# Kernel optimization log

Hardware: AMD Instinct MI355X
Metric: run time of the kernel (lower is better)

## Reference

```python
import jax, jax.numpy as jnp
import numpy as np

VOCAB = 100000
EMB = 128
WINDOW = 200
N_T = 64
B = 128
N_W = 128
ALPHA = 0.5
PAD = VOCAB - 1


def setup_inputs() -> dict:
    key = jax.random.key(0)
    ks = jax.random.split(key, 8)
    s = 0.5 / EMB
    tvecs = jax.random.uniform(ks[0], (VOCAB, EMB), minval=-s, maxval=s).at[PAD].set(0.0)
    cvecs = jax.random.uniform(ks[1], (VOCAB, EMB), minval=-s, maxval=s).at[PAD].set(0.0)
    W_w = jax.random.normal(ks[2], (N_W, 2 * EMB)) * 0.02
    W_b = jnp.zeros((N_W,))
    h_w = jax.random.normal(ks[3], (1, N_W)) * 0.02
    h_b = jnp.zeros((1,))
    batch_titems = jax.random.randint(ks[4], (B, N_T), 0, VOCAB)
    batch_citems = jax.random.randint(ks[5], (B, WINDOW), 0, VOCAB)
    mask_pad_ids = jax.random.randint(ks[6], (B, WINDOW), 0, 2).astype(bool)
    return {
        "tvecs": tvecs, "cvecs": cvecs,
        "W_w": W_w, "W_b": W_b, "h_w": h_w, "h_b": h_b,
        "batch_titems": batch_titems, "batch_citems": batch_citems,
        "mask_pad_ids": mask_pad_ids,
    }


def reference(tvecs, cvecs, W_w, W_b, h_w, h_b, batch_titems, batch_citems, mask_pad_ids):
    q = tvecs[batch_titems]   # (B, N_T, E)  target-item (query) embeddings
    k = cvecs[batch_citems]   # (B, W, E)    context-item (key/value) embeddings
    # W(concat(p, q)) == p @ Wp.T + q @ Wq.T + b  -- split weight, avoid the
    # materialized (B, N_T, W, 2E) repeat+cat tensor of the torch code.
    Wp, Wq = W_w[:, :EMB], W_w[:, EMB:]
    hp = jnp.einsum('bte,ne->btn', q, Wp)   # (B, N_T, N_W)
    hq = jnp.einsum('bwe,ne->bwn', k, Wq)   # (B, W,  N_W)
    hidden = jax.nn.relu(hp[:, :, None, :] + hq[:, None, :, :] + W_b)  # (B,N_T,W,N_W)
    att = jnp.einsum('btwn,n->btw', hidden, h_w[0]) + h_b[0]            # (B,N_T,W)
    att = jnp.where(mask_pad_ids[:, None, :], -jnp.inf, att)
    att = jax.nn.softmax(att, axis=-1)
    out = jnp.einsum('btw,bwe->bte', att, k)                            # (B,N_T,E)
    norm = (1000.0 - mask_pad_ids.sum(axis=1).astype(out.dtype)) ** ALPHA  # (B,)
    return out / norm[:, None, None]
```

## Files before the change

kernel.cpp:

```cpp
#include <hip/hip_runtime.h>
#include <math.h>

#define EMB 128
#define WIN 200
#define NT 64
#define BB 128
#define WPAD 208

typedef short bf16x8 __attribute__((ext_vector_type(8)));
typedef float f32x4  __attribute__((ext_vector_type(4)));

__device__ __forceinline__ unsigned pk2bf16(float a, float b) {
    unsigned ua = __float_as_uint(a), ub = __float_as_uint(b);
    ua = (ua + 0x7FFFu + ((ua >> 16) & 1u)) >> 16;
    ub = (ub + 0x7FFFu + ((ub >> 16) & 1u)) >> 16;
    return ua | (ub << 16);
}
__device__ __forceinline__ float rdlane(float v, int l) {
    return __uint_as_float(__builtin_amdgcn_readlane(__float_as_uint(v), l));
}

__global__ __launch_bounds__(256, 4) void proj_kernel(
    const float* __restrict__ tvecs, const float* __restrict__ cvecs,
    const int* __restrict__ titems, const int* __restrict__ citems,
    const float* __restrict__ Ww, const float* __restrict__ Wbias,
    const int* __restrict__ mi, int* __restrict__ flag,
    float* __restrict__ hp_out, float* __restrict__ hqT_out)
{
    __shared__ __align__(16) ushort s_A[64 * 128];
    __shared__ __align__(16) ushort s_B[128 * 128];
    __shared__ float s_bias[128];
    __shared__ int   sdet;

    const int tid = threadIdx.x;

    if (blockIdx.x == 528) {
        if (tid == 0) sdet = 0;
        __syncthreads();
        int bad = 0;
        for (int i = tid; i < 6400; i += 256)
            if ((unsigned)mi[i] > 1u) bad = 1;
        if (bad) sdet = 1;
        __syncthreads();
        if (tid == 0) flag[0] = sdet;
        return;
    }

    const bool is_hp = blockIdx.x < 128;
    const float* table = is_hp ? tvecs : cvecs;
    const int*   idx   = is_hp ? titems : citems;
    const int  rbase = (is_hp ? blockIdx.x : (blockIdx.x - 128)) * 64;
    const int  eoff  = is_hp ? 0 : EMB;

    if (tid < 128) s_bias[tid] = Wbias[tid];

    for (int i = tid; i < 2048; i += 256) {
        int row = i >> 5, j = i & 31;
        float4 v = *(const float4*)&table[(size_t)idx[rbase + row] * 128 + 4 * j];
        uint2 p; p.x = pk2bf16(v.x, v.y); p.y = pk2bf16(v.z, v.w);
        *(uint2*)((char*)s_A + row * 256 + (((j >> 1) ^ (row & 7)) << 4) + (j & 1) * 8) = p;
    }
    for (int i = tid; i < 4096; i += 256) {
        int n = i >> 5, j = i & 31;
        float4 v = *(const float4*)&Ww[n * 256 + eoff + 4 * j];
        uint2 p; p.x = pk2bf16(v.x, v.y); p.y = pk2bf16(v.z, v.w);
        *(uint2*)((char*)s_B + n * 256 + (((j >> 1) ^ (n & 7)) << 4) + (j & 1) * 8) = p;
    }
    __syncthreads();

    const int wid = tid >> 6, l = tid & 63;
    const int rl = l & 15, kg = l >> 4;
    const int r0 = wid * 16;

    f32x4 acc[8];
#pragma unroll
    for (int i = 0; i < 8; ++i) acc[i] = (f32x4){0.f, 0.f, 0.f, 0.f};

    const int arow = r0 + rl;
#pragma unroll
    for (int s = 0; s < 4; ++s) {
        bf16x8 af = *(const bf16x8*)((const char*)s_A
                        + arow * 256 + ((((s << 2) + kg) ^ (arow & 7)) << 4));
#pragma unroll
        for (int nt = 0; nt < 8; ++nt) {
            int bn = nt * 16 + rl;
            bf16x8 bfr = *(const bf16x8*)((const char*)s_B
                            + bn * 256 + ((((s << 2) + kg) ^ (bn & 7)) << 4));
            acc[nt] = __builtin_amdgcn_mfma_f32_16x16x32_bf16(af, bfr, acc[nt], 0, 0, 0);
        }
    }

#pragma unroll
    for (int i = 0; i < 4; ++i) {
        int ri = rbase + r0 + kg * 4 + i;
        if (is_hp) {
            size_t base = (size_t)ri * 128;
#pragma unroll
            for (int nt = 0; nt < 8; ++nt)
                hp_out[base + nt * 16 + rl] = acc[nt][i];
        } else {
            int b2 = ri / 200;
            int wl = ri - b2 * 200;
#pragma unroll
            for (int nt = 0; nt < 8; ++nt) {
                int col = nt * 16 + rl;
                hqT_out[(((size_t)b2 * 32 + (col >> 2)) * WPAD + wl) * 4 + (col & 3)]
                    = acc[nt][i] + s_bias[col];
            }
        }
    }
}

__global__ __launch_bounds__(512, 2) void attn_kernel(
    const float* __restrict__ cvecs, const int* __restrict__ citems,
    const void* __restrict__ mask_raw, const int* __restrict__ flagp,
    const float* __restrict__ hwg, const float* __restrict__ hp,
    const float* __restrict__ hqT, float* __restrict__ outp)
{
    __shared__ __align__(16) float4 s_hq4[32 * 128];
    __shared__ __align__(16) float4 s_k4[128 * 32];
    __shared__ __align__(16) float  s_hp[32 * 128];
    __shared__ __align__(16) float  s_hw[128];
    __shared__ int s_ci[WIN];
    __shared__ int s_widx[WIN];
    __shared__ int s_m;

    const int tid  = threadIdx.x;
    const int b    = blockIdx.x >> 1;
    const int tb   = (blockIdx.x & 1) * 32;
    const int lane = tid & 63;
    const int wid  = tid >> 6;
    const int t0   = wid * 4;

    for (int i = tid; i < 1024; i += 512) {
        int t = i >> 5, e4 = i & 31;
        *(float4*)&s_hp[t * 128 + e4 * 4] =
            *(const float4*)&hp[((size_t)(b * 64 + tb + t)) * 128 + e4 * 4];
    }
    if (tid < 128) s_hw[tid] = hwg[tid];
    if (tid < WIN) s_ci[tid] = citems[b * WIN + tid];
    if (wid == 0) {
        const int boolmode = flagp[0];
        const unsigned char* mb = (const unsigned char*)mask_raw;
        const int*           mi = (const int*)mask_raw;
        int base = 0;
#pragma unroll
        for (int r = 0; r < 4; ++r) {
            int w  = r * 64 + lane;
            int mv = 1;
            if (w < WIN) mv = boolmode ? (int)mb[b * WIN + w] : mi[b * WIN + w];
            unsigned long long act = __ballot(mv == 0);
            if (mv == 0)
                s_widx[base + __popcll(act & ((1ull << lane) - 1ull))] = w;
            base += __popcll(act);
        }
        if (lane == 0) s_m = base;
    }
    __syncthreads();

    const int m = s_m;
    const float invn = 1.f / sqrtf(800.f + (float)m);
    size_t orow = ((size_t)(b * 64 + tb + t0)) * 128;

    if (m == 0) {
#pragma unroll
        for (int j = 0; j < 4; ++j)
            *(float2*)&outp[orow + (size_t)j * 128 + lane * 2] = make_float2(0.f, 0.f);
        return;
    }

    const float4* hq4  = (const float4*)hqT + (size_t)b * 32 * WPAD;
    const float4* hp4a = (const float4*)&s_hp[t0 * 128];
    const float4* hw4p = (const float4*)s_hw;
    const float4* cv4  = (const float4*)cvecs;

#define SC(J, K, HV, P)                                                        \
    va[J][K] += hwv.x * fmaxf(HV.x + P.x, 0.f) + hwv.y * fmaxf(HV.y + P.y, 0.f)\
              + hwv.z * fmaxf(HV.z + P.z, 0.f) + hwv.w * fmaxf(HV.w + P.w, 0.f);

    if (m <= 128) {
        {
            const int w2 = tid & 127, nc0 = tid >> 7;
            if (w2 < m) {
                const int wi = s_widx[w2];
#pragma unroll
                for (int nc = nc0; nc < 32; nc += 4)
                    s_hq4[nc * 128 + w2] = hq4[(size_t)nc * WPAD + wi];
            }
            const int e4 = tid & 31, w0 = tid >> 5;
            for (int w2k = w0; w2k < m; w2k += 16) {
                int ci = s_ci[s_widx[w2k]];
                s_k4[w2k * 32 + e4] = cv4[(size_t)ci * 32 + e4];
            }
        }
        __syncthreads();

        float va[4][2];
#pragma unroll
        for (int j = 0; j < 4; ++j) { va[j][0] = 0.f; va[j][1] = 0.f; }

#pragma unroll 2
        for (int nc = 0; nc < 32; ++nc) {
            float4 hv0 = s_hq4[nc * 128 + lane];
            float4 hv1 = s_hq4[nc * 128 + 64 + lane];
            float4 hwv = hw4p[nc];
            float4 p0  = hp4a[0 * 32 + nc];
            float4 p1  = hp4a[1 * 32 + nc];
            float4 p2  = hp4a[2 * 32 + nc];
            float4 p3  = hp4a[3 * 32 + nc];
            SC(0, 0, hv0, p0) SC(0, 1, hv1, p0)
            SC(1, 0, hv0, p1) SC(1, 1, hv1, p1)
            SC(2, 0, hv0, p2) SC(2, 1, hv1, p2)
            SC(3, 0, hv0, p3) SC(3, 1, hv1, p3)
        }

#pragma unroll
        for (int j = 0; j < 4; ++j) {
            float mx = -1e30f;
#pragma unroll
            for (int kt = 0; kt < 2; ++kt) {
                float v = (kt * 64 + lane < m) ? va[j][kt] : -1e30f;
                va[j][kt] = v;
                mx = fmaxf(mx, v);
            }
#pragma unroll
            for (int off = 32; off; off >>= 1) mx = fmaxf(mx, __shfl_xor(mx, off));
            float sum = 0.f;
#pragma unroll
            for (int kt = 0; kt < 2; ++kt) {
                float e = (va[j][kt] <= -1e29f) ? 0.f : __expf(va[j][kt] - mx);
                va[j][kt] = e;
                sum += e;
            }
#pragma unroll
            for (int off = 32; off; off >>= 1) sum += __shfl_xor(sum, off);
            float is = 1.f / sum;
            va[j][0] *= is; va[j][1] *= is;
        }

        float2 po[4];
#pragma unroll
        for (int j = 0; j < 4; ++j) po[j] = make_float2(0.f, 0.f);
        const float2* s_k2 = (const float2*)s_k4;
#pragma unroll
        for (int kt = 0; kt < 2; ++kt) {
            if (kt * 64 < m) {
                const int wn = min(64, m - kt * 64);
                for (int w = 0; w < wn; ++w) {
                    float2 kv = s_k2[(kt * 64 + w) * 64 + lane];
                    float a0 = rdlane(va[0][kt], w);
                    float a1 = rdlane(va[1][kt], w);
                    float a2 = rdlane(va[2][kt], w);
                    float a3 = rdlane(va[3][kt], w);
                    po[0].x += a0 * kv.x; po[0].y += a0 * kv.y;
                    po[1].x += a1 * kv.x; po[1].y += a1 * kv.y;
                    po[2].x += a2 * kv.x; po[2].y += a2 * kv.y;
                    po[3].x += a3 * kv.x; po[3].y += a3 * kv.y;
                }
            }
        }
#pragma unroll
        for (int j = 0; j < 4; ++j)
            *(float2*)&outp[orow + (size_t)j * 128 + lane * 2] =
                make_float2(po[j].x * invn, po[j].y * invn);
    } else {
        int wreg[4];
        const int mc = m - 1;
#pragma unroll
        for (int kt = 0; kt < 4; ++kt)
            wreg[kt] = s_widx[min(kt * 64 + lane, mc)];

        float va[4][4];
#pragma unroll
        for (int j = 0; j < 4; ++j)
#pragma unroll
            for (int k = 0; k < 4; ++k) va[j][k] = 0.f;

#pragma unroll 2
        for (int nc = 0; nc < 32; ++nc) {
            const float4* base = hq4 + (size_t)nc * WPAD;
            float4 hv0 = base[wreg[0]];
            float4 hv1 = base[wreg[1]];
            float4 hv2 = base[wreg[2]];
            float4 hv3 = base[wreg[3]];
            float4 hwv = hw4p[nc];
            float4 p0  = hp4a[0 * 32 + nc];
            float4 p1  = hp4a[1 * 32 + nc];
            float4 p2  = hp4a[2 * 32 + nc];
            float4 p3  = hp4a[3 * 32 + nc];
            SC(0, 0, hv0, p0) SC(0, 1, hv1, p0) SC(0, 2, hv2, p0) SC(0, 3, hv3, p0)
            SC(1, 0, hv0, p1) SC(1, 1, hv1, p1) SC(1, 2, hv2, p1) SC(1, 3, hv3, p1)
            SC(2, 0, hv0, p2) SC(2, 1, hv1, p2) SC(2, 2, hv2, p2) SC(2, 3, hv3, p2)
            SC(3, 0, hv0, p3) SC(3, 1, hv1, p3) SC(3, 2, hv2, p3) SC(3, 3, hv3, p3)
        }

#pragma unroll
        for (int j = 0; j < 4; ++j) {
            float mx = -1e30f;
#pragma unroll
            for (int kt = 0; kt < 4; ++kt) {
                float v = (kt * 64 + lane < m) ? va[j][kt] : -1e30f;
                va[j][kt] = v;
                mx = fmaxf(mx, v);
            }
#pragma unroll
            for (int off = 32; off; off >>= 1) mx = fmaxf(mx, __shfl_xor(mx, off));
            float sum = 0.f;
#pragma unroll
            for (int kt = 0; kt < 4; ++kt) {
                float e = (va[j][kt] <= -1e29f) ? 0.f : __expf(va[j][kt] - mx);
                va[j][kt] = e;
                sum += e;
            }
#pragma unroll
            for (int off = 32; off; off >>= 1) sum += __shfl_xor(sum, off);
            float is = 1.f / sum;
#pragma unroll
            for (int kt = 0; kt < 4; ++kt) va[j][kt] *= is;
        }

        float2 po[4];
#pragma unroll
        for (int j = 0; j < 4; ++j) po[j] = make_float2(0.f, 0.f);
        const char* cvb = (const char*)cvecs;
#pragma unroll
        for (int kt = 0; kt < 4; ++kt) {
            if (kt * 64 < m) {
                const int wn = min(64, m - kt * 64);
                for (int w = 0; w < wn; ++w) {
                    unsigned off = (unsigned)s_ci[s_widx[kt * 64 + w]] * 512u;
                    float2 kv = *(const float2*)(cvb + off + lane * 8);
                    float a0 = rdlane(va[0][kt], w);
                    float a1 = rdlane(va[1][kt], w);
                    float a2 = rdlane(va[2][kt], w);
                    float a3 = rdlane(va[3][kt], w);
                    po[0].x += a0 * kv.x; po[0].y += a0 * kv.y;
                    po[1].x += a1 * kv.x; po[1].y += a1 * kv.y;
                    po[2].x += a2 * kv.x; po[2].y += a2 * kv.y;
                    po[3].x += a3 * kv.x; po[3].y += a3 * kv.y;
                }
            }
        }
#pragma unroll
        for (int j = 0; j < 4; ++j)
            *(float2*)&outp[orow + (size_t)j * 128 + lane * 2] =
                make_float2(po[j].x * invn, po[j].y * invn);
    }
#undef SC
}

extern "C" void kernel_launch(void* const* d_in, const int* in_sizes, int n_in,
                              void* d_out, int out_size, void* d_ws, size_t ws_size,
                              hipStream_t stream) {
    const float* tvecs = (const float*)d_in[0];
    const float* cvecs = (const float*)d_in[1];
    const float* Ww    = (const float*)d_in[2];
    const float* Wb    = (const float*)d_in[3];
    const float* hw    = (const float*)d_in[4];
    const int* titems  = (const int*)d_in[6];
    const int* citems  = (const int*)d_in[7];
    const void* mask   = d_in[8];
    float* out         = (float*)d_out;

    const size_t needed = (size_t)(64 + (size_t)BB * NT * 128
                                   + (size_t)BB * 32 * WPAD * 4) * 4;
    if (ws_size < needed) return;

    int*   flag   = (int*)d_ws;
    float* hp_ws  = (float*)d_ws + 64;
    float* hqT_ws = hp_ws + (size_t)BB * NT * 128;

    proj_kernel<<<529, 256, 0, stream>>>(tvecs, cvecs, titems, citems,
                                         Ww, Wb, (const int*)mask, flag,
                                         hp_ws, hqT_ws);
    attn_kernel<<<BB * 2, 512, 0, stream>>>(cvecs, citems, mask, flag,
                                            hw, hp_ws, hqT_ws, out);
}
```

Baseline: 51.99 us.

## Store projection intermediates and staged keys as bf16, enlarge proj blocks

The projection outputs hp and hqT are now written to workspace as bf16 instead of fp32. The attention kernel reads them as bf16, stages context key vectors in shared memory as bf16, and unpacks everything to fp32 for the math. The projection kernel moves to 512-thread blocks that each handle 128 rows, and the attention kernel's launch bounds are raised to 4 blocks. This halves intermediate memory traffic and LDS use to allow more occupancy, but adds rounding error in the scores and the output.

```diff
diff --git a/kernel.cpp b/kernel.cpp
--- a/kernel.cpp
+++ b/kernel.cpp
@@ -10,35 +10,41 @@
 typedef short bf16x8 __attribute__((ext_vector_type(8)));
 typedef float f32x4  __attribute__((ext_vector_type(4)));
 
+__device__ __forceinline__ ushort bf16r(float x) {
+    unsigned u = __float_as_uint(x);
+    return (ushort)((u + 0x7FFFu + ((u >> 16) & 1u)) >> 16);
+}
 __device__ __forceinline__ unsigned pk2bf16(float a, float b) {
     unsigned ua = __float_as_uint(a), ub = __float_as_uint(b);
     ua = (ua + 0x7FFFu + ((ua >> 16) & 1u)) >> 16;
     ub = (ub + 0x7FFFu + ((ub >> 16) & 1u)) >> 16;
     return ua | (ub << 16);
 }
+__device__ __forceinline__ float bf_lo(unsigned u) { return __uint_as_float(u << 16); }
+__device__ __forceinline__ float bf_hi(unsigned u) { return __uint_as_float(u & 0xFFFF0000u); }
 __device__ __forceinline__ float rdlane(float v, int l) {
     return __uint_as_float(__builtin_amdgcn_readlane(__float_as_uint(v), l));
 }
 
-__global__ __launch_bounds__(256, 4) void proj_kernel(
+__global__ __launch_bounds__(512, 4) void proj_kernel(
     const float* __restrict__ tvecs, const float* __restrict__ cvecs,
     const int* __restrict__ titems, const int* __restrict__ citems,
     const float* __restrict__ Ww, const float* __restrict__ Wbias,
     const int* __restrict__ mi, int* __restrict__ flag,
-    float* __restrict__ hp_out, float* __restrict__ hqT_out)
+    ushort* __restrict__ hp_out, ushort* __restrict__ hqT_out)
 {
-    __shared__ __align__(16) ushort s_A[64 * 128];
+    __shared__ __align__(16) ushort s_A[128 * 128];
     __shared__ __align__(16) ushort s_B[128 * 128];
     __shared__ float s_bias[128];
     __shared__ int   sdet;
 
     const int tid = threadIdx.x;
 
-    if (blockIdx.x == 528) {
+    if (blockIdx.x == 264) {
         if (tid == 0) sdet = 0;
         __syncthreads();
         int bad = 0;
-        for (int i = tid; i < 6400; i += 256)
+        for (int i = tid; i < 6400; i += 512)
             if ((unsigned)mi[i] > 1u) bad = 1;
         if (bad) sdet = 1;
         __syncthreads();
@@ -46,21 +52,21 @@
         return;
     }
 
-    const bool is_hp = blockIdx.x < 128;
+    const bool is_hp = blockIdx.x < 64;
     const float* table = is_hp ? tvecs : cvecs;
     const int*   idx   = is_hp ? titems : citems;
-    const int  rbase = (is_hp ? blockIdx.x : (blockIdx.x - 128)) * 64;
+    const int  rbase = (is_hp ? blockIdx.x : (blockIdx.x - 64)) * 128;
     const int  eoff  = is_hp ? 0 : EMB;
 
     if (tid < 128) s_bias[tid] = Wbias[tid];
 
-    for (int i = tid; i < 2048; i += 256) {
+    for (int i = tid; i < 4096; i += 512) {
         int row = i >> 5, j = i & 31;
         float4 v = *(const float4*)&table[(size_t)idx[rbase + row] * 128 + 4 * j];
         uint2 p; p.x = pk2bf16(v.x, v.y); p.y = pk2bf16(v.z, v.w);
         *(uint2*)((char*)s_A + row * 256 + (((j >> 1) ^ (row & 7)) << 4) + (j & 1) * 8) = p;
     }
-    for (int i = tid; i < 4096; i += 256) {
+    for (int i = tid; i < 4096; i += 512) {
         int n = i >> 5, j = i & 31;
         float4 v = *(const float4*)&Ww[n * 256 + eoff + 4 * j];
         uint2 p; p.x = pk2bf16(v.x, v.y); p.y = pk2bf16(v.z, v.w);
@@ -97,7 +103,7 @@
             size_t base = (size_t)ri * 128;
 #pragma unroll
             for (int nt = 0; nt < 8; ++nt)
-                hp_out[base + nt * 16 + rl] = acc[nt][i];
+                hp_out[base + nt * 16 + rl] = bf16r(acc[nt][i]);
         } else {
             int b2 = ri / 200;
             int wl = ri - b2 * 200;
@@ -105,22 +111,22 @@
             for (int nt = 0; nt < 8; ++nt) {
                 int col = nt * 16 + rl;
                 hqT_out[(((size_t)b2 * 32 + (col >> 2)) * WPAD + wl) * 4 + (col & 3)]
-                    = acc[nt][i] + s_bias[col];
-            }
-        }
-    }
-}
-
-__global__ __launch_bounds__(512, 2) void attn_kernel(
+                    = bf16r(acc[nt][i] + s_bias[col]);
+            }
+        }
+    }
+}
+
+__global__ __launch_bounds__(512, 4) void attn_kernel(
     const float* __restrict__ cvecs, const int* __restrict__ citems,
     const void* __restrict__ mask_raw, const int* __restrict__ flagp,
-    const float* __restrict__ hwg, const float* __restrict__ hp,
-    const float* __restrict__ hqT, float* __restrict__ outp)
+    const float* __restrict__ hwg, const ushort* __restrict__ hp16,
+    const ushort* __restrict__ hqT16, float* __restrict__ outp)
 {
-    __shared__ __align__(16) float4 s_hq4[32 * 128];
-    __shared__ __align__(16) float4 s_k4[128 * 32];
-    __shared__ __align__(16) float  s_hp[32 * 128];
-    __shared__ __align__(16) float  s_hw[128];
+    __shared__ __align__(16) uint2  s_hq2[32 * 128];
+    __shared__ __align__(16) ushort s_k[128 * 128];
+    __shared__ __align__(16) ushort s_hp[32 * 128];
+    __shared__ float s_hw[128];
     __shared__ int s_ci[WIN];
     __shared__ int s_widx[WIN];
     __shared__ int s_m;
@@ -132,11 +138,8 @@
     const int wid  = tid >> 6;
     const int t0   = wid * 4;
 
-    for (int i = tid; i < 1024; i += 512) {
-        int t = i >> 5, e4 = i & 31;
-        *(float4*)&s_hp[t * 128 + e4 * 4] =
-            *(const float4*)&hp[((size_t)(b * 64 + tb + t)) * 128 + e4 * 4];
-    }
+    for (int i = tid; i < 1024; i += 512)
+        ((uint2*)s_hp)[i] = ((const uint2*)hp16)[((size_t)(b * 64 + tb)) * 32 + i];
     if (tid < 128) s_hw[tid] = hwg[tid];
     if (tid < WIN) s_ci[tid] = citems[b * WIN + tid];
     if (wid == 0) {
@@ -169,28 +172,29 @@
         return;
     }
 
-    const float4* hq4  = (const float4*)hqT + (size_t)b * 32 * WPAD;
-    const float4* hp4a = (const float4*)&s_hp[t0 * 128];
+    const uint2* hq2g = (const uint2*)hqT16;
     const float4* hw4p = (const float4*)s_hw;
-    const float4* cv4  = (const float4*)cvecs;
-
-#define SC(J, K, HV, P)                                                        \
-    va[J][K] += hwv.x * fmaxf(HV.x + P.x, 0.f) + hwv.y * fmaxf(HV.y + P.y, 0.f)\
-              + hwv.z * fmaxf(HV.z + P.z, 0.f) + hwv.w * fmaxf(HV.w + P.w, 0.f);
+    const int mc = m - 1;
+
+#define SCB(J, K, HA, HB, HC, HD)                                              \
+    va[J][K] += hwv.x * fmaxf(HA + pa, 0.f) + hwv.y * fmaxf(HB + pb, 0.f)      \
+              + hwv.z * fmaxf(HC + pc, 0.f) + hwv.w * fmaxf(HD + pd, 0.f);
 
     if (m <= 128) {
+        for (int i = tid; i < 4096; i += 512) {
+            int nc = i >> 7, w2 = i & 127;
+            if (w2 < m)
+                s_hq2[nc * 128 + w2] = hq2g[(size_t)(b * 32 + nc) * WPAD + s_widx[w2]];
+        }
         {
-            const int w2 = tid & 127, nc0 = tid >> 7;
-            if (w2 < m) {
-                const int wi = s_widx[w2];
-#pragma unroll
-                for (int nc = nc0; nc < 32; nc += 4)
-                    s_hq4[nc * 128 + w2] = hq4[(size_t)nc * WPAD + wi];
-            }
-            const int e4 = tid & 31, w0 = tid >> 5;
-            for (int w2k = w0; w2k < m; w2k += 16) {
-                int ci = s_ci[s_widx[w2k]];
-                s_k4[w2k * 32 + e4] = cv4[(size_t)ci * 32 + e4];
+            const int er = tid & 15, wr = tid >> 4;
+            for (int w2 = wr; w2 < m; w2 += 32) {
+                const float4* src = (const float4*)&cvecs[(size_t)s_ci[s_widx[w2]] * 128 + er * 8];
+                float4 a = src[0], c = src[1];
+                uint4 p;
+                p.x = pk2bf16(a.x, a.y); p.y = pk2bf16(a.z, a.w);
+                p.z = pk2bf16(c.x, c.y); p.w = pk2bf16(c.z, c.w);
+                *(uint4*)&s_k[w2 * 128 + er * 8] = p;
             }
         }
         __syncthreads();
@@ -201,17 +205,18 @@
 
 #pragma unroll 2
         for (int nc = 0; nc < 32; ++nc) {
-            float4 hv0 = s_hq4[nc * 128 + lane];
-            float4 hv1 = s_hq4[nc * 128 + 64 + lane];
+            uint2 h0 = s_hq2[nc * 128 + lane];
+            uint2 h1 = s_hq2[nc * 128 + 64 + lane];
+            float h0a = bf_lo(h0.x), h0b = bf_hi(h0.x), h0c = bf_lo(h0.y), h0d = bf_hi(h0.y);
+            float h1a = bf_lo(h1.x), h1b = bf_hi(h1.x), h1c = bf_lo(h1.y), h1d = bf_hi(h1.y);
             float4 hwv = hw4p[nc];
-            float4 p0  = hp4a[0 * 32 + nc];
-            float4 p1  = hp4a[1 * 32 + nc];
-            float4 p2  = hp4a[2 * 32 + nc];
-            float4 p3  = hp4a[3 * 32 + nc];
-            SC(0, 0, hv0, p0) SC(0, 1, hv1, p0)
-            SC(1, 0, hv0, p1) SC(1, 1, hv1, p1)
-            SC(2, 0, hv0, p2) SC(2, 1, hv1, p2)
-            SC(3, 0, hv0, p3) SC(3, 1, hv1, p3)
+#pragma unroll
+            for (int jt = 0; jt < 4; ++jt) {
+                uint2 pu = *(const uint2*)&s_hp[(t0 + jt) * 128 + nc * 4];
+                float pa = bf_lo(pu.x), pb = bf_hi(pu.x), pc = bf_lo(pu.y), pd = bf_hi(pu.y);
+                SCB(jt, 0, h0a, h0b, h0c, h0d)
+                SCB(jt, 1, h1a, h1b, h1c, h1d)
+            }
         }
 
 #pragma unroll
@@ -241,21 +246,21 @@
         float2 po[4];
 #pragma unroll
         for (int j = 0; j < 4; ++j) po[j] = make_float2(0.f, 0.f);
-        const float2* s_k2 = (const float2*)s_k4;
 #pragma unroll
         for (int kt = 0; kt < 2; ++kt) {
             if (kt * 64 < m) {
                 const int wn = min(64, m - kt * 64);
                 for (int w = 0; w < wn; ++w) {
-                    float2 kv = s_k2[(kt * 64 + w) * 64 + lane];
+                    unsigned ku = *(const unsigned*)&s_k[(kt * 64 + w) * 128 + lane * 2];
+                    float kx = bf_lo(ku), ky = bf_hi(ku);
                     float a0 = rdlane(va[0][kt], w);
                     float a1 = rdlane(va[1][kt], w);
                     float a2 = rdlane(va[2][kt], w);
                     float a3 = rdlane(va[3][kt], w);
-                    po[0].x += a0 * kv.x; po[0].y += a0 * kv.y;
-                    po[1].x += a1 * kv.x; po[1].y += a1 * kv.y;
-                    po[2].x += a2 * kv.x; po[2].y += a2 * kv.y;
-                    po[3].x += a3 * kv.x; po[3].y += a3 * kv.y;
+                    po[0].x += a0 * kx; po[0].y += a0 * ky;
+                    po[1].x += a1 * kx; po[1].y += a1 * ky;
+                    po[2].x += a2 * kx; po[2].y += a2 * ky;
+                    po[3].x += a3 * kx; po[3].y += a3 * ky;
                 }
             }
         }
@@ -265,7 +270,6 @@
                 make_float2(po[j].x * invn, po[j].y * invn);
     } else {
         int wreg[4];
-        const int mc = m - 1;
 #pragma unroll
         for (int kt = 0; kt < 4; ++kt)
             wreg[kt] = s_widx[min(kt * 64 + lane, mc)];
@@ -278,20 +282,24 @@
 
 #pragma unroll 2
         for (int nc = 0; nc < 32; ++nc) {
-            const float4* base = hq4 + (size_t)nc * WPAD;
-            float4 hv0 = base[wreg[0]];
-            float4 hv1 = base[wreg[1]];
-            float4 hv2 = base[wreg[2]];
-            float4 hv3 = base[wreg[3]];
+            const uint2* base = hq2g + (size_t)(b * 32 + nc) * WPAD;
+            float h[4][4];
+#pragma unroll
+            for (int kt = 0; kt < 4; ++kt) {
+                uint2 hu = base[wreg[kt]];
+                h[kt][0] = bf_lo(hu.x); h[kt][1] = bf_hi(hu.x);
+                h[kt][2] = bf_lo(hu.y); h[kt][3] = bf_hi(hu.y);
+            }
             float4 hwv = hw4p[nc];
-            float4 p0  = hp4a[0 * 32 + nc];
-            float4 p1  = hp4a[1 * 32 + nc];
-            float4 p2  = hp4a[2 * 32 + nc];
-            float4 p3  = hp4a[3 * 32 + nc];
-            SC(0, 0, hv0, p0) SC(0, 1, hv1, p0) SC(0, 2, hv2, p0) SC(0, 3, hv3, p0)
-            SC(1, 0, hv0, p1) SC(1, 1, hv1, p1) SC(1, 2, hv2, p1) SC(1, 3, hv3, p1)
-            SC(2, 0, hv0, p2) SC(2, 1, hv1, p2) SC(2, 2, hv2, p2) SC(2, 3, hv3, p2)
-            SC(3, 0, hv0, p3) SC(3, 1, hv1, p3) SC(3, 2, hv2, p3) SC(3, 3, hv3, p3)
+#pragma unroll
+            for (int jt = 0; jt < 4; ++jt) {
+                uint2 pu = *(const uint2*)&s_hp[(t0 + jt) * 128 + nc * 4];
+                float pa = bf_lo(pu.x), pb = bf_hi(pu.x), pc = bf_lo(pu.y), pd = bf_hi(pu.y);
+                SCB(jt, 0, h[0][0], h[0][1], h[0][2], h[0][3])
+                SCB(jt, 1, h[1][0], h[1][1], h[1][2], h[1][3])
+                SCB(jt, 2, h[2][0], h[2][1], h[2][2], h[2][3])
+                SCB(jt, 3, h[3][0], h[3][1], h[3][2], h[3][3])
+            }
         }
 
 #pragma unroll
@@ -346,7 +354,7 @@
             *(float2*)&outp[orow + (size_t)j * 128 + lane * 2] =
                 make_float2(po[j].x * invn, po[j].y * invn);
     }
-#undef SC
+#undef SCB
 }
 
 extern "C" void kernel_launch(void* const* d_in, const int* in_sizes, int n_in,
@@ -362,17 +370,18 @@
     const void* mask   = d_in[8];
     float* out         = (float*)d_out;
 
-    const size_t needed = (size_t)(64 + (size_t)BB * NT * 128
-                                   + (size_t)BB * 32 * WPAD * 4) * 4;
+    const size_t hp_elems  = (size_t)BB * NT * 128;
+    const size_t hq_elems  = (size_t)BB * 32 * WPAD * 4;
+    const size_t needed = 256 + hp_elems * 2 + hq_elems * 2;
     if (ws_size < needed) return;
 
-    int*   flag   = (int*)d_ws;
-    float* hp_ws  = (float*)d_ws + 64;
-    float* hqT_ws = hp_ws + (size_t)BB * NT * 128;
-
-    proj_kernel<<<529, 256, 0, stream>>>(tvecs, cvecs, titems, citems,
+    int*    flag   = (int*)d_ws;
+    ushort* hp16   = (ushort*)((char*)d_ws + 256);
+    ushort* hqT16  = hp16 + hp_elems;
+
+    proj_kernel<<<265, 512, 0, stream>>>(tvecs, cvecs, titems, citems,
                                          Ww, Wb, (const int*)mask, flag,
-                                         hp_ws, hqT_ws);
+                                         hp16, hqT16);
     attn_kernel<<<BB * 2, 512, 0, stream>>>(cvecs, citems, mask, flag,
-                                            hw, hp_ws, hqT_ws, out);
-}
+                                            hw, hp16, hqT16, out);
+}
```

Result: faster. 50.42 us (-3.0%).

## Store hq row-major, double proj tile rows, swizzle attention block order

Applied to the files above, without the earlier changes.

The projection kernel now processes 128 rows per 512-thread block instead of 64 per 256-thread block, halving the grid. The hq workspace changes from a padded transposed layout to plain row-major, so the attention kernel gathers each context row's 32 float4 values contiguously. Attention blocks are remapped with a bid swizzle to spread batches across CUs. The row-major layout makes the proj stores coalesced but changes the access pattern of the m>128 path's per-lane gathers, which may now stride across rows.

```diff
diff --git a/kernel.cpp b/kernel.cpp
--- a/kernel.cpp
+++ b/kernel.cpp
@@ -5,7 +5,6 @@
 #define WIN 200
 #define NT 64
 #define BB 128
-#define WPAD 208
 
 typedef short bf16x8 __attribute__((ext_vector_type(8)));
 typedef float f32x4  __attribute__((ext_vector_type(4)));
@@ -20,25 +19,25 @@
     return __uint_as_float(__builtin_amdgcn_readlane(__float_as_uint(v), l));
 }
 
-__global__ __launch_bounds__(256, 4) void proj_kernel(
+__global__ __launch_bounds__(512, 4) void proj_kernel(
     const float* __restrict__ tvecs, const float* __restrict__ cvecs,
     const int* __restrict__ titems, const int* __restrict__ citems,
     const float* __restrict__ Ww, const float* __restrict__ Wbias,
     const int* __restrict__ mi, int* __restrict__ flag,
-    float* __restrict__ hp_out, float* __restrict__ hqT_out)
+    float* __restrict__ hp_out, float* __restrict__ hq_out)
 {
-    __shared__ __align__(16) ushort s_A[64 * 128];
+    __shared__ __align__(16) ushort s_A[128 * 128];
     __shared__ __align__(16) ushort s_B[128 * 128];
     __shared__ float s_bias[128];
     __shared__ int   sdet;
 
     const int tid = threadIdx.x;
 
-    if (blockIdx.x == 528) {
+    if (blockIdx.x == 264) {
         if (tid == 0) sdet = 0;
         __syncthreads();
         int bad = 0;
-        for (int i = tid; i < 6400; i += 256)
+        for (int i = tid; i < 6400; i += 512)
             if ((unsigned)mi[i] > 1u) bad = 1;
         if (bad) sdet = 1;
         __syncthreads();
@@ -46,21 +45,21 @@
         return;
     }
 
-    const bool is_hp = blockIdx.x < 128;
+    const bool is_hp = blockIdx.x < 64;
     const float* table = is_hp ? tvecs : cvecs;
     const int*   idx   = is_hp ? titems : citems;
-    const int  rbase = (is_hp ? blockIdx.x : (blockIdx.x - 128)) * 64;
+    const int  rbase = (is_hp ? blockIdx.x : (blockIdx.x - 64)) * 128;
     const int  eoff  = is_hp ? 0 : EMB;
 
     if (tid < 128) s_bias[tid] = Wbias[tid];
 
-    for (int i = tid; i < 2048; i += 256) {
+    for (int i = tid; i < 4096; i += 512) {
         int row = i >> 5, j = i & 31;
         float4 v = *(const float4*)&table[(size_t)idx[rbase + row] * 128 + 4 * j];
         uint2 p; p.x = pk2bf16(v.x, v.y); p.y = pk2bf16(v.z, v.w);
         *(uint2*)((char*)s_A + row * 256 + (((j >> 1) ^ (row & 7)) << 4) + (j & 1) * 8) = p;
     }
-    for (int i = tid; i < 4096; i += 256) {
+    for (int i = tid; i < 4096; i += 512) {
         int n = i >> 5, j = i & 31;
         float4 v = *(const float4*)&Ww[n * 256 + eoff + 4 * j];
         uint2 p; p.x = pk2bf16(v.x, v.y); p.y = pk2bf16(v.z, v.w);
@@ -92,20 +91,16 @@
 
 #pragma unroll
     for (int i = 0; i < 4; ++i) {
-        int ri = rbase + r0 + kg * 4 + i;
+        size_t base = (size_t)(rbase + r0 + kg * 4 + i) * 128;
         if (is_hp) {
-            size_t base = (size_t)ri * 128;
 #pragma unroll
             for (int nt = 0; nt < 8; ++nt)
                 hp_out[base + nt * 16 + rl] = acc[nt][i];
         } else {
-            int b2 = ri / 200;
-            int wl = ri - b2 * 200;
 #pragma unroll
             for (int nt = 0; nt < 8; ++nt) {
                 int col = nt * 16 + rl;
-                hqT_out[(((size_t)b2 * 32 + (col >> 2)) * WPAD + wl) * 4 + (col & 3)]
-                    = acc[nt][i] + s_bias[col];
+                hq_out[base + col] = acc[nt][i] + s_bias[col];
             }
         }
     }
@@ -115,7 +110,7 @@
     const float* __restrict__ cvecs, const int* __restrict__ citems,
     const void* __restrict__ mask_raw, const int* __restrict__ flagp,
     const float* __restrict__ hwg, const float* __restrict__ hp,
-    const float* __restrict__ hqT, float* __restrict__ outp)
+    const float* __restrict__ hq, float* __restrict__ outp)
 {
     __shared__ __align__(16) float4 s_hq4[32 * 128];
     __shared__ __align__(16) float4 s_k4[128 * 32];
@@ -126,8 +121,10 @@
     __shared__ int s_m;
 
     const int tid  = threadIdx.x;
-    const int b    = blockIdx.x >> 1;
-    const int tb   = (blockIdx.x & 1) * 32;
+    const int bid  = blockIdx.x;
+    const int swz  = (bid & 7) * 32 + (bid >> 3);
+    const int b    = swz >> 1;
+    const int tb   = (swz & 1) * 32;
     const int lane = tid & 63;
     const int wid  = tid >> 6;
     const int t0   = wid * 4;
@@ -169,7 +166,7 @@
         return;
     }
 
-    const float4* hq4  = (const float4*)hqT + (size_t)b * 32 * WPAD;
+    const float4* hq4r = (const float4*)hq + (size_t)b * 200 * 32;
     const float4* hp4a = (const float4*)&s_hp[t0 * 128];
     const float4* hw4p = (const float4*)s_hw;
     const float4* cv4  = (const float4*)cvecs;
@@ -185,7 +182,7 @@
                 const int wi = s_widx[w2];
 #pragma unroll
                 for (int nc = nc0; nc < 32; nc += 4)
-                    s_hq4[nc * 128 + w2] = hq4[(size_t)nc * WPAD + wi];
+                    s_hq4[nc * 128 + w2] = hq4r[(size_t)wi * 32 + nc];
             }
             const int e4 = tid & 31, w0 = tid >> 5;
             for (int w2k = w0; w2k < m; w2k += 16) {
@@ -278,11 +275,10 @@
 
 #pragma unroll 2
         for (int nc = 0; nc < 32; ++nc) {
-            const float4* base = hq4 + (size_t)nc * WPAD;
-            float4 hv0 = base[wreg[0]];
-            float4 hv1 = base[wreg[1]];
-            float4 hv2 = base[wreg[2]];
-            float4 hv3 = base[wreg[3]];
+            float4 hv0 = hq4r[(size_t)wreg[0] * 32 + nc];
+            float4 hv1 = hq4r[(size_t)wreg[1] * 32 + nc];
+            float4 hv2 = hq4r[(size_t)wreg[2] * 32 + nc];
+            float4 hv3 = hq4r[(size_t)wreg[3] * 32 + nc];
             float4 hwv = hw4p[nc];
             float4 p0  = hp4a[0 * 32 + nc];
             float4 p1  = hp4a[1 * 32 + nc];
@@ -362,17 +358,18 @@
     const void* mask   = d_in[8];
     float* out         = (float*)d_out;
 
-    const size_t needed = (size_t)(64 + (size_t)BB * NT * 128
-                                   + (size_t)BB * 32 * WPAD * 4) * 4;
+    const size_t hp_elems = (size_t)BB * NT * 128;
+    const size_t hq_elems = (size_t)BB * WIN * 128;
+    const size_t needed = 256 + (hp_elems + hq_elems) * 4;
     if (ws_size < needed) return;
 
-    int*   flag   = (int*)d_ws;
-    float* hp_ws  = (float*)d_ws + 64;
-    float* hqT_ws = hp_ws + (size_t)BB * NT * 128;
-
-    proj_kernel<<<529, 256, 0, stream>>>(tvecs, cvecs, titems, citems,
+    int*   flag  = (int*)d_ws;
+    float* hp_ws = (float*)((char*)d_ws + 256);
+    float* hq_ws = hp_ws + hp_elems;
+
+    proj_kernel<<<265, 512, 0, stream>>>(tvecs, cvecs, titems, citems,
                                          Ww, Wb, (const int*)mask, flag,
-                                         hp_ws, hqT_ws);
+                                         hp_ws, hq_ws);
     attn_kernel<<<BB * 2, 512, 0, stream>>>(cvecs, citems, mask, flag,
-                                            hw, hp_ws, hqT_ws, out);
-}
+                                            hw, hp_ws, hq_ws, out);
+}
```

Measured after the change: 48.20 us. 1.08x faster.
